# Kernel optimization log

Hardware: AMD Instinct MI355X
Metric: run time of the kernel (lower is better)

The kernel has to match this reference:

```python
import jax, jax.numpy as jnp
import numpy as np

DECAY = 0.99
EPS = 1e-06


def setup_inputs() -> dict:
    key = jax.random.key(0)
    k0, k1, k2, k3 = jax.random.split(key, 4)
    B, D, h, w = 1024, 64, 8, 8
    K, L = 512, h * w
    inp = jax.random.normal(k0, (B, D, h, w), dtype=jnp.float32)
    embedding = 0.01 * jax.random.normal(k1, (D, K, L), dtype=jnp.float32)
    dw = 0.01 * jax.random.normal(k2, (D, K, L), dtype=jnp.float32)
    cluster_size = 10.0 * jax.random.uniform(k3, (K, L), dtype=jnp.float32)
    return {"input": inp, "embedding": embedding, "dw": dw, "cluster_size": cluster_size}


def reference(input, embedding, dw, cluster_size):
    B, D, h, w = input.shape
    L = h * w
    K = embedding.shape[1]
    x = input.reshape(B, D, L)  # [B, D, L]

    # nearest-code assignment: argmin_k ||e[:,k,l] - x[b,:,l]||
    # ||x||^2 is constant over k, so argmin of ||e||^2 - 2<x,e> is equivalent
    e2 = jnp.sum(embedding * embedding, axis=0)              # [K, L]
    xe = jnp.einsum('bdl,dkl->bkl', x, embedding)            # [B, K, L]
    d2 = e2[None, :, :] - 2.0 * xe                           # [B, K, L]
    encoding_indices = jnp.argmin(d2, axis=1)                # [B, L]
    encoding = jax.nn.one_hot(encoding_indices, K, axis=1, dtype=x.dtype)  # [B, K, L]

    # decode: gather per-latent codebook entries (independent codebooks)
    emb_lkd = jnp.transpose(embedding, (2, 1, 0))            # [L, K, D]
    q = emb_lkd[jnp.arange(L)[None, :], encoding_indices]    # [B, L, D]
    q = jnp.transpose(q, (0, 2, 1))                          # [B, D, L]

    # EMA bookkeeping (training branch, independent_codebook=True)
    n = jnp.sum(cluster_size, axis=-1, keepdims=True) + 1e-06          # [K, 1]
    cs = (cluster_size + EPS) / (n + K * EPS) * n                      # [K, L]
    cs = DECAY * cs + (1.0 - DECAY) * jnp.sum(encoding, axis=0)        # [K, L]
    dw_batch = jnp.einsum('bkl,bdl->dkl', encoding, x)                 # [D, K, L]
    avg_probs = jnp.mean(encoding, axis=0)                             # [K, L]
    perplexity = jnp.exp(-jnp.sum(avg_probs * jnp.log(avg_probs + 1e-10), axis=0)) / K  # [L]
    dw_buf = DECAY * dw + (1.0 - DECAY) * (dw_batch / cs[None, :, :])  # [D, K, L]
    emb_new = DECAY * embedding + (1.0 - DECAY) * dw_buf               # [D, K, L]

    commitment_loss = jnp.mean((q - x) ** 2)
    quantized = (x + (q - x)).reshape(B, D, h, w)  # straight-through (value == q)
    encoding_out = encoding.reshape(B, K, h, w)
    return quantized, encoding_out, commitment_loss, perplexity, emb_new, dw_buf, cs
```

## Files before the change

kernel.cpp:

```cpp
#include <hip/hip_runtime.h>


typedef float f32x4 __attribute__((ext_vector_type(4)));

__global__ __launch_bounds__(256) void ktransAll(const float* __restrict__ emb,
                                                 const float* __restrict__ x,
                                                 float* __restrict__ eT,
                                                 float* __restrict__ e2T,
                                                 float* __restrict__ xT,
                                                 float* __restrict__ countsT,
                                                 double* __restrict__ lossAcc) {
  const int t = threadIdx.x;
  __shared__ float s[64][65];
  if (blockIdx.x < 512) {
    const int k = blockIdx.x;
#pragma unroll
    for (int i = 0; i < 16; ++i) {
      int e = t + i * 256;
      int d = e >> 6, l = e & 63;
      s[d][l] = emb[d * 32768 + k * 64 + l];
    }
    __syncthreads();
    if (t < 64) {
      float s2 = 0.f;
#pragma unroll
      for (int d = 0; d < 64; ++d) {
        float v = s[d][t];
        s2 = __fadd_rn(s2, __fmul_rn(v, v));
      }
      e2T[t * 512 + k] = s2;
      countsT[k * 64 + t] = 0.f;
    }
    if (k == 0 && t == 0) lossAcc[0] = 0.0;
#pragma unroll
    for (int i = 0; i < 4; ++i) {
      int j = t + i * 256;
      int l = j >> 4, d0 = (j & 15) * 4;
      float4 w;
      w.x = s[d0][l]; w.y = s[d0 + 1][l]; w.z = s[d0 + 2][l]; w.w = s[d0 + 3][l];
      *(float4*)&eT[(l * 512 + k) * 64 + d0] = w;
    }
  } else {
    const int b = blockIdx.x - 512;
    const float* xp = x + b * 4096;
#pragma unroll
    for (int i = 0; i < 4; ++i) {
      int f4 = t + i * 256;
      float4 v = *(const float4*)&xp[f4 * 4];
      int d = f4 >> 4, l0 = (f4 & 15) * 4;
      s[d][l0] = v.x; s[d][l0 + 1] = v.y; s[d][l0 + 2] = v.z; s[d][l0 + 3] = v.w;
    }
    __syncthreads();
#pragma unroll
    for (int i = 0; i < 4; ++i) {
      int j = t + i * 256;
      int l = j >> 4, d0 = (j & 15) * 4;
      float4 w;
      w.x = s[d0][l]; w.y = s[d0 + 1][l]; w.z = s[d0 + 2][l]; w.w = s[d0 + 3][l];
      *(float4*)&xT[((size_t)l * 1024 + b) * 64 + d0] = w;
    }
  }
}

__global__ __launch_bounds__(256, 2) void kargmin(const float* __restrict__ xT,
                                                  const float* __restrict__ eT,
                                                  const float* __restrict__ e2T,
                                                  int* __restrict__ idxout,
                                                  int* __restrict__ idxTout,
                                                  float* __restrict__ countsT) {
  const int l = blockIdx.x;
  const int b0 = blockIdx.y * 128;
  const int t = threadIdx.x;
  __shared__ float xs[128][68];
  __shared__ float es[128][68];
  __shared__ float e2s[128];
  const float* xsrc = xT + ((size_t)l * 1024 + b0) * 64;
#pragma unroll
  for (int i = 0; i < 8; ++i) {
    int f4 = t + i * 256;
    int r = f4 >> 4;
    int c = (f4 & 15) * 4;
    *(float4*)&xs[r][c] = *(const float4*)&xsrc[f4 * 4];
  }
  const int bg = t & 15;
  const int kg = t >> 4;
  float bestv[8];
  int bestk[8];
#pragma unroll
  for (int i = 0; i < 8; ++i) { bestv[i] = 3.4e38f; bestk[i] = 0; }

  for (int chunk = 0; chunk < 4; ++chunk) {
    __syncthreads();
    const float* src = eT + (l * 512 + chunk * 128) * 64;
#pragma unroll
    for (int i = 0; i < 8; ++i) {
      int f4 = t + i * 256;
      int r = f4 >> 4;
      int c = (f4 & 15) * 4;
      *(float4*)&es[r][c] = *(const float4*)&src[f4 * 4];
    }
    if (t < 128) e2s[t] = e2T[l * 512 + chunk * 128 + t];
    __syncthreads();

    float acc[8][8];
#pragma unroll
    for (int i = 0; i < 8; ++i)
#pragma unroll
      for (int j = 0; j < 8; ++j) acc[i][j] = 0.f;

    for (int d4 = 0; d4 < 16; ++d4) {
      float4 xv[8], ev[8];
#pragma unroll
      for (int i = 0; i < 8; ++i) xv[i] = *(const float4*)&xs[bg + i * 16][d4 * 4];
#pragma unroll
      for (int j = 0; j < 8; ++j) ev[j] = *(const float4*)&es[kg + j * 16][d4 * 4];
#pragma unroll
      for (int i = 0; i < 8; ++i)
#pragma unroll
        for (int j = 0; j < 8; ++j) {
          acc[i][j] = fmaf(xv[i].x, ev[j].x, acc[i][j]);
          acc[i][j] = fmaf(xv[i].y, ev[j].y, acc[i][j]);
          acc[i][j] = fmaf(xv[i].z, ev[j].z, acc[i][j]);
          acc[i][j] = fmaf(xv[i].w, ev[j].w, acc[i][j]);
        }
    }
#pragma unroll
    for (int j = 0; j < 8; ++j) {
      int kk = kg + j * 16;
      int kglob = chunk * 128 + kk;
      float e2v = e2s[kk];
#pragma unroll
      for (int i = 0; i < 8; ++i) {
        float d2 = fmaf(-2.0f, acc[i][j], e2v);
        if (d2 < bestv[i] || (d2 == bestv[i] && kglob < bestk[i])) {
          bestv[i] = d2; bestk[i] = kglob;
        }
      }
    }
  }
  __syncthreads();
  float* rv = &es[0][0];
  float* rkf = &xs[0][0];
#pragma unroll
  for (int i = 0; i < 8; ++i) {
    int bl = bg + i * 16;
    rv[bl * 16 + kg] = bestv[i];
    rkf[bl * 16 + kg] = (float)bestk[i];
  }
  __syncthreads();
  if (t < 128) {
    float bv = rv[t * 16];
    int bk = (int)rkf[t * 16];
#pragma unroll
    for (int g = 1; g < 16; ++g) {
      float v = rv[t * 16 + g];
      int kk = (int)rkf[t * 16 + g];
      if (v < bv || (v == bv && kk < bk)) { bv = v; bk = kk; }
    }
    idxout[(b0 + t) * 64 + l] = bk;
    idxTout[l * 1024 + b0 + t] = bk;
    unsafeAtomicAdd(&countsT[l * 512 + bk], 1.0f);
  }
}

__global__ __launch_bounds__(256) void kdwgather(const float* __restrict__ x,
                                                 const float* __restrict__ xT,
                                                 const float* __restrict__ eT,
                                                 const int* __restrict__ idxb,
                                                 const int* __restrict__ idxT,
                                                 float* __restrict__ dwT,
                                                 float* __restrict__ out_q,
                                                 float* __restrict__ out_enc,
                                                 double* __restrict__ lossAcc) {
  const int t = threadIdx.x;
  __shared__ float SM[8192];
  if (blockIdx.x < 256) {
    const int l = blockIdx.x & 63;
    const int kq = (blockIdx.x >> 6) * 128;
    float* acc = SM;
#pragma unroll
    for (int i = 0; i < 32; ++i) acc[t + i * 256] = 0.f;
    const int w = t >> 6, lane = t & 63;
    __syncthreads();
    const int* idxl = idxT + l * 1024;
    const float* xTl = xT + (size_t)l * 65536;
    for (int c = 0; c < 4; ++c) {
      const int base = w * 256 + c * 64;
      const int myidx = idxl[base + lane];
      for (int jj = 0; jj < 64; jj += 8) {
        int ks[8]; float vs[8];
#pragma unroll
        for (int u = 0; u < 8; ++u) ks[u] = __shfl(myidx, jj + u, 64) - kq;
#pragma unroll
        for (int u = 0; u < 8; ++u)
          if ((unsigned)ks[u] < 128u)
            vs[u] = xTl[(size_t)(base + jj + u) * 64 + lane];
#pragma unroll
        for (int u = 0; u < 8; ++u)
          if ((unsigned)ks[u] < 128u)
            atomicAdd(&acc[(ks[u] << 6) + lane], vs[u]);
      }
    }
    __syncthreads();
#pragma unroll
    for (int i = 0; i < 32; ++i) {
      int e = t + i * 256;
      int k = e >> 6, d = e & 63;
      dwT[((size_t)(kq + k) * 64 + l) * 64 + d] = acc[e];
    }
  } else {
    const int b = blockIdx.x - 256;
    float (*qb)[68] = (float (*)[68])SM;
    int* lidx = (int*)(SM + 4352);
    double* wsumS = (double*)(SM + 4432);
    if (t < 64) lidx[t] = idxb[b * 64 + t];
    __syncthreads();
    const int l = t >> 2, qd = (t & 3) * 16;
    const int kse = lidx[l];
    const float* ep = eT + (l * 512 + kse) * 64 + qd;
#pragma unroll
    for (int j = 0; j < 4; ++j) {
      float4 v = *(const float4*)&ep[j * 4];
      qb[qd + j * 4 + 0][l] = v.x;
      qb[qd + j * 4 + 1][l] = v.y;
      qb[qd + j * 4 + 2][l] = v.z;
      qb[qd + j * 4 + 3][l] = v.w;
    }
    __syncthreads();
    float ls = 0.f;
    const float* xp = x + b * 4096;
    float* op = out_q + b * 4096;
#pragma unroll
    for (int i = 0; i < 4; ++i) {
      int f4 = t + i * 256;
      float4 xv = *(const float4*)&xp[f4 * 4];
      int d = f4 >> 4, l0 = (f4 & 15) * 4;
      float4 qv = *(const float4*)&qb[d][l0];
      f32x4 ov;
      float dx = qv.x - xv.x, dy = qv.y - xv.y, dz = qv.z - xv.z, dw_ = qv.w - xv.w;
      ov.x = xv.x + dx; ov.y = xv.y + dy; ov.z = xv.z + dz; ov.w = xv.w + dw_;
      __builtin_nontemporal_store(ov, (f32x4*)&op[f4 * 4]);
      ls = fmaf(dx, dx, ls); ls = fmaf(dy, dy, ls);
      ls = fmaf(dz, dz, ls); ls = fmaf(dw_, dw_, ls);
    }
    float* encp = out_enc + (size_t)b * 32768;
#pragma unroll
    for (int i = 0; i < 32; ++i) {
      int f4 = t + i * 256;
      int e = f4 * 4;
      int k = e >> 6, l0 = e & 63;
      f32x4 v;
      v.x = (lidx[l0 + 0] == k) ? 1.f : 0.f;
      v.y = (lidx[l0 + 1] == k) ? 1.f : 0.f;
      v.z = (lidx[l0 + 2] == k) ? 1.f : 0.f;
      v.w = (lidx[l0 + 3] == k) ? 1.f : 0.f;
      __builtin_nontemporal_store(v, (f32x4*)&encp[e]);
    }
#pragma unroll
    for (int off = 32; off > 0; off >>= 1) ls += __shfl_down(ls, off, 64);
    if ((t & 63) == 0) wsumS[t >> 6] = (double)ls;
    __syncthreads();
    if (t == 0) unsafeAtomicAdd(lossAcc, wsumS[0] + wsumS[1] + wsumS[2] + wsumS[3]);
  }
}

__global__ __launch_bounds__(256) void kemafinal(const float* __restrict__ cluster,
                                                 const float* __restrict__ countsT,
                                                 const float* __restrict__ dw,
                                                 const float* __restrict__ emb,
                                                 const float* __restrict__ dwT,
                                                 const double* __restrict__ lossAcc,
                                                 float* __restrict__ out_cs,
                                                 float* __restrict__ out_emb,
                                                 float* __restrict__ out_dwb,
                                                 float* __restrict__ out_loss,
                                                 float* __restrict__ out_perp) {
  const int t = threadIdx.x;
  if (blockIdx.x >= 512) {
    const int l = blockIdx.x - 512;
    if (t < 64) {
      float s = 0.f;
#pragma unroll
      for (int i = 0; i < 8; ++i) {
        int k = t * 8 + i;
        float p = countsT[l * 512 + k] * (1.0f / 1024.0f);
        s = __fadd_rn(s, __fmul_rn(p, logf(__fadd_rn(p, 1e-10f))));
      }
#pragma unroll
      for (int off = 32; off > 0; off >>= 1) s += __shfl_down(s, off, 64);
      if (t == 0) out_perp[l] = expf(-s) * (1.0f / 512.0f);
    }
    if (blockIdx.x == 512 && t == 64)
      out_loss[0] = (float)(lossAcc[0] / 4194304.0);
    return;
  }
  const int k = blockIdx.x;
  __shared__ float dwS[64][65];
  __shared__ float csS[64];
  __shared__ float nS;
  const float* sp = dwT + (size_t)k * 4096;
#pragma unroll
  for (int i = 0; i < 4; ++i) {
    int f4 = t + i * 256;
    float4 v = *(const float4*)&sp[f4 * 4];
    int l = f4 >> 4, d0 = (f4 & 15) * 4;
    dwS[l][d0] = v.x; dwS[l][d0 + 1] = v.y; dwS[l][d0 + 2] = v.z; dwS[l][d0 + 3] = v.w;
  }
  const float* cp = cluster + k * 64;
  if (t == 0) {
    float n = 0.f;
#pragma unroll
    for (int l = 0; l < 64; ++l) n = __fadd_rn(n, cp[l]);
    nS = __fadd_rn(n, 1e-06f);
  }
  __syncthreads();
  if (t < 64) {
    const float n = nS;
    const float denom = __fadd_rn(n, 0.000512f);
    float t1 = __fadd_rn(cp[t], 1e-06f);
    float r = __fdiv_rn(t1, denom);
    float r2 = __fmul_rn(r, n);
    float cs = __fadd_rn(__fmul_rn(0.99f, r2), __fmul_rn(0.01f, countsT[t * 512 + k]));
    csS[t] = cs;
    out_cs[k * 64 + t] = cs;
  }
  __syncthreads();
  const int l = t & 63;
  const int dlane = t >> 6;
#pragma unroll
  for (int r = 0; r < 16; ++r) {
    int d = r * 4 + dlane;
    int g = d * 32768 + k * 64 + l;
    float batch = dwS[l][d];
    float buf = 0.99f * dw[g] + 0.01f * (batch / csS[l]);
    out_dwb[g] = buf;
    out_emb[g] = 0.99f * emb[g] + 0.01f * buf;
  }
}

extern "C" void kernel_launch(void* const* d_in, const int* in_sizes, int n_in,
                              void* d_out, int out_size, void* d_ws, size_t ws_size,
                              hipStream_t stream) {
  (void)in_sizes; (void)n_in; (void)out_size; (void)ws_size;
  const float* x    = (const float*)d_in[0];
  const float* emb  = (const float*)d_in[1];
  const float* dw   = (const float*)d_in[2];
  const float* clus = (const float*)d_in[3];

  float* out = (float*)d_out;
  float* out_q    = out;
  float* out_enc  = out + 4194304;
  float* out_loss = out + 37748736;
  float* out_perp = out + 37748737;
  float* out_emb  = out + 37748801;
  float* out_dwb  = out + 39845953;
  float* out_cs   = out + 41943105;

  float* wsf = (float*)d_ws;
  float*  dwT     = wsf;
  float*  countsT = wsf + 2097152;
  float*  eT      = wsf + 2129920;
  float*  e2T     = wsf + 4227072;
  int*    idxb    = (int*)(wsf + 4259840);
  int*    idxT    = (int*)(wsf + 4325376);
  double* lossA   = (double*)(wsf + 4390912);
  float*  xT      = wsf + 4456448;

  ktransAll<<<1536, 256, 0, stream>>>(emb, x, eT, e2T, xT, countsT, lossA);
  kargmin<<<dim3(64, 8), 256, 0, stream>>>(xT, eT, e2T, idxb, idxT, countsT);
  kdwgather<<<1280, 256, 0, stream>>>(x, xT, eT, idxb, idxT, dwT, out_q, out_enc, lossA);
  kemafinal<<<576, 256, 0, stream>>>(clus, countsT, dw, emb, dwT, lossA,
                                     out_cs, out_emb, out_dwb, out_loss, out_perp);
}
```

Baseline: 133.1 us.

## Replace LDS-tiled argmin GEMM with register-resident x and wave-uniform codebook reads

Rewrites the argmin kernel so each lane holds one batch row's 64-dim x vector in registers, and each wave scans a 128-code slice of the codebook. The codebook is read with wave-uniform addresses, which can become scalar loads. This removes the shared-memory tiling and the per-chunk syncthreads, and launches twice as many blocks. In exchange each codebook element is reused only across 64 lanes rather than through an 8x8 register tile, and global/scalar cache traffic rises. Tie-breaking within a wave now relies on sequential strict-less comparisons.

```diff
diff --git a/kernel.cpp b/kernel.cpp
--- a/kernel.cpp
+++ b/kernel.cpp
@@ -62,100 +62,61 @@
   }
 }
 
-__global__ __launch_bounds__(256, 2) void kargmin(const float* __restrict__ xT,
-                                                  const float* __restrict__ eT,
-                                                  const float* __restrict__ e2T,
-                                                  int* __restrict__ idxout,
-                                                  int* __restrict__ idxTout,
-                                                  float* __restrict__ countsT) {
+__global__ __launch_bounds__(256) void kargmin_s(const float* __restrict__ xT,
+                                                 const float* __restrict__ eT,
+                                                 const float* __restrict__ e2T,
+                                                 int* __restrict__ idxout,
+                                                 int* __restrict__ idxTout,
+                                                 float* __restrict__ countsT) {
   const int l = blockIdx.x;
-  const int b0 = blockIdx.y * 128;
+  const int b0 = blockIdx.y * 64;
   const int t = threadIdx.x;
-  __shared__ float xs[128][68];
-  __shared__ float es[128][68];
-  __shared__ float e2s[128];
-  const float* xsrc = xT + ((size_t)l * 1024 + b0) * 64;
-#pragma unroll
-  for (int i = 0; i < 8; ++i) {
-    int f4 = t + i * 256;
-    int r = f4 >> 4;
-    int c = (f4 & 15) * 4;
-    *(float4*)&xs[r][c] = *(const float4*)&xsrc[f4 * 4];
-  }
-  const int bg = t & 15;
-  const int kg = t >> 4;
-  float bestv[8];
-  int bestk[8];
-#pragma unroll
-  for (int i = 0; i < 8; ++i) { bestv[i] = 3.4e38f; bestk[i] = 0; }
-
-  for (int chunk = 0; chunk < 4; ++chunk) {
-    __syncthreads();
-    const float* src = eT + (l * 512 + chunk * 128) * 64;
-#pragma unroll
-    for (int i = 0; i < 8; ++i) {
-      int f4 = t + i * 256;
-      int r = f4 >> 4;
-      int c = (f4 & 15) * 4;
-      *(float4*)&es[r][c] = *(const float4*)&src[f4 * 4];
-    }
-    if (t < 128) e2s[t] = e2T[l * 512 + chunk * 128 + t];
-    __syncthreads();
-
-    float acc[8][8];
-#pragma unroll
-    for (int i = 0; i < 8; ++i)
-#pragma unroll
-      for (int j = 0; j < 8; ++j) acc[i][j] = 0.f;
-
-    for (int d4 = 0; d4 < 16; ++d4) {
-      float4 xv[8], ev[8];
-#pragma unroll
-      for (int i = 0; i < 8; ++i) xv[i] = *(const float4*)&xs[bg + i * 16][d4 * 4];
-#pragma unroll
-      for (int j = 0; j < 8; ++j) ev[j] = *(const float4*)&es[kg + j * 16][d4 * 4];
-#pragma unroll
-      for (int i = 0; i < 8; ++i)
-#pragma unroll
-        for (int j = 0; j < 8; ++j) {
-          acc[i][j] = fmaf(xv[i].x, ev[j].x, acc[i][j]);
-          acc[i][j] = fmaf(xv[i].y, ev[j].y, acc[i][j]);
-          acc[i][j] = fmaf(xv[i].z, ev[j].z, acc[i][j]);
-          acc[i][j] = fmaf(xv[i].w, ev[j].w, acc[i][j]);
-        }
-    }
-#pragma unroll
-    for (int j = 0; j < 8; ++j) {
-      int kk = kg + j * 16;
-      int kglob = chunk * 128 + kk;
-      float e2v = e2s[kk];
-#pragma unroll
-      for (int i = 0; i < 8; ++i) {
-        float d2 = fmaf(-2.0f, acc[i][j], e2v);
-        if (d2 < bestv[i] || (d2 == bestv[i] && kglob < bestk[i])) {
-          bestv[i] = d2; bestk[i] = kglob;
-        }
-      }
-    }
-  }
+  const int lane = t & 63;
+  const int w = __builtin_amdgcn_readfirstlane(t >> 6);
+  __shared__ float rv[4][64];
+  __shared__ float rkf[4][64];
+
+  float4 xr[16];
+  const float4* xp = (const float4*)(xT + ((size_t)l * 1024 + b0 + lane) * 64);
+#pragma unroll
+  for (int i = 0; i < 16; ++i) xr[i] = xp[i];
+
+  const float* __restrict__ ew = eT + ((size_t)l * 512 + w * 128) * 64;
+  const float* __restrict__ e2w = e2T + l * 512 + w * 128;
+  float bestv = 3.4e38f;
+  int bestk = 0;
+
+  for (int kk = 0; kk < 128; kk += 2) {
+    const float* e0 = ew + kk * 64;
+    const float* e1 = e0 + 64;
+    float a0 = 0.f, a1 = 0.f;
+#pragma unroll
+    for (int i = 0; i < 16; ++i) {
+      a0 = fmaf(xr[i].x, e0[i * 4 + 0], a0);
+      a0 = fmaf(xr[i].y, e0[i * 4 + 1], a0);
+      a0 = fmaf(xr[i].z, e0[i * 4 + 2], a0);
+      a0 = fmaf(xr[i].w, e0[i * 4 + 3], a0);
+      a1 = fmaf(xr[i].x, e1[i * 4 + 0], a1);
+      a1 = fmaf(xr[i].y, e1[i * 4 + 1], a1);
+      a1 = fmaf(xr[i].z, e1[i * 4 + 2], a1);
+      a1 = fmaf(xr[i].w, e1[i * 4 + 3], a1);
+    }
+    float d0 = fmaf(-2.0f, a0, e2w[kk]);
+    float d1 = fmaf(-2.0f, a1, e2w[kk + 1]);
+    if (d0 < bestv) { bestv = d0; bestk = w * 128 + kk; }
+    if (d1 < bestv) { bestv = d1; bestk = w * 128 + kk + 1; }
+  }
+  rv[w][lane] = bestv;
+  rkf[w][lane] = (float)bestk;
   __syncthreads();
-  float* rv = &es[0][0];
-  float* rkf = &xs[0][0];
-#pragma unroll
-  for (int i = 0; i < 8; ++i) {
-    int bl = bg + i * 16;
-    rv[bl * 16 + kg] = bestv[i];
-    rkf[bl * 16 + kg] = (float)bestk[i];
-  }
-  __syncthreads();
-  if (t < 128) {
-    float bv = rv[t * 16];
-    int bk = (int)rkf[t * 16];
-#pragma unroll
-    for (int g = 1; g < 16; ++g) {
-      float v = rv[t * 16 + g];
-      int kk = (int)rkf[t * 16 + g];
-      if (v < bv || (v == bv && kk < bk)) { bv = v; bk = kk; }
+  if (t < 64) {
+    float bv = rv[0][t];
+    int bk = (int)rkf[0][t];
+#pragma unroll
+    for (int g = 1; g < 4; ++g) {
+      float v = rv[g][t];
+      int kk2 = (int)rkf[g][t];
+      if (v < bv || (v == bv && kk2 < bk)) { bv = v; bk = kk2; }
     }
     idxout[(b0 + t) * 64 + l] = bk;
     idxTout[l * 1024 + b0 + t] = bk;
@@ -367,7 +328,7 @@
   float*  xT      = wsf + 4456448;
 
   ktransAll<<<1536, 256, 0, stream>>>(emb, x, eT, e2T, xT, countsT, lossA);
-  kargmin<<<dim3(64, 8), 256, 0, stream>>>(xT, eT, e2T, idxb, idxT, countsT);
+  kargmin_s<<<dim3(64, 16), 256, 0, stream>>>(xT, eT, e2T, idxb, idxT, countsT);
   kdwgather<<<1280, 256, 0, stream>>>(x, xT, eT, idxb, idxT, dwT, out_q, out_enc, lossA);
   kemafinal<<<576, 256, 0, stream>>>(clus, countsT, dw, emb, dwT, lossA,
                                      out_cs, out_emb, out_dwb, out_loss, out_perp);
```

Measured after the change: 171.4 us. +28.7%, slower.
